# Kernel tuning notes

Hardware: AMD Instinct MI355X
Metric: run time of the kernel (lower is better)

Reference implementation:

```python
import jax, jax.numpy as jnp
import numpy as np

B, H, W = 128, 48, 48
CEN_IN, CEN_OUT, DIR_IN, DIR_OUT, CEN_K, DIR_K = 32, 32, 24, 24, 3, 5
C_IN = CEN_IN + 4 * DIR_IN  # central + 4 directional groups (hor, ver, diag, anti-diag)


def _dwconv(x, k):
    # x: [B, C, H, W], k: [C, kh, kw] depthwise kernels -> SAME-padded depthwise conv
    C = x.shape[1]
    return jax.lax.conv_general_dilated(
        x, k[:, None], window_strides=(1, 1), padding='SAME',
        dimension_numbers=('NCHW', 'OIHW', 'NCHW'), feature_group_count=C)


def setup_inputs() -> dict:
    key = jax.random.key(0)
    ks = jax.random.split(key, 8)
    s = 0.1
    return {
        'x': jax.random.normal(ks[0], (B, C_IN, H, W), dtype=jnp.float32),
        'cen_tensor': jax.random.normal(ks[1], (CEN_IN, CEN_K, CEN_K), dtype=jnp.float32) * s,
        'dir_tensor': jax.random.normal(ks[2], (DIR_IN, DIR_K), dtype=jnp.float32) * s,
        'cen2cen': jax.random.normal(ks[3], (CEN_OUT, CEN_IN), dtype=jnp.float32) * s,
        'par2cen': jax.random.normal(ks[4], (CEN_OUT, DIR_IN), dtype=jnp.float32) * s,
        'dia2cen': jax.random.normal(ks[5], (CEN_OUT, DIR_IN), dtype=jnp.float32) * s,
        'cen2dir': jax.random.normal(ks[6], (DIR_OUT, CEN_IN), dtype=jnp.float32) * s,
        'dir2dir': jax.random.normal(ks[7], (DIR_OUT, DIR_IN), dtype=jnp.float32) * s,
    }


def reference(x, cen_tensor, dir_tensor, cen2cen, par2cen, dia2cen, cen2dir, dir2dir):
    cen_in = cen_tensor.shape[0]
    dir_in, K = dir_tensor.shape
    # split channel groups: [cen | hor | ver | diag | anti-diag]
    xc = x[:, :cen_in]
    xh = x[:, cen_in:cen_in + dir_in]
    xv = x[:, cen_in + dir_in:cen_in + 2 * dir_in]
    xd1 = x[:, cen_in + 2 * dir_in:cen_in + 3 * dir_in]
    xd2 = x[:, cen_in + 3 * dir_in:]
    eye = jnp.eye(K, dtype=x.dtype)
    # --- directional depthwise stage ---
    yc = _dwconv(xc, cen_tensor)                                # full 2D kernel per channel
    yh = _dwconv(xh, dir_tensor[:, None, :])
    yv = _dwconv(xv, dir_tensor[:, :, None])                    # K x 1 vertical line
    yd1 = _dwconv(xd1, dir_tensor[:, :, None] * eye)            # main diagonal line
    yd2 = _dwconv(xd2, dir_tensor[:, :, None] * eye[:, ::-1])   # anti-diagonal line
    # --- directional pointwise (1x1) mixing stage ---
    mix = lambda Wm, t: jnp.einsum('oc,bchw->bohw', Wm, t)
    out_cen = mix(cen2cen, yc) + mix(par2cen, yh + yv) + mix(dia2cen, yd1 + yd2)
    od_cen = mix(cen2dir, yc)
    out_dirs = [od_cen + mix(dir2dir, t) for t in (yh, yv, yd1, yd2)]
    return jnp.concatenate([out_cen] + out_dirs, axis=1)
```

## Files before the change

kernel.cpp:

```cpp
#include <hip/hip_runtime.h>
#include <hip/hip_bf16.h>


namespace {
constexpr int HH = 48, WW = 48, HW = HH * WW;
constexpr int C_IN = 128, C_OUT = 128, NB = 128;
constexpr int RPB = 8;
constexpr int NSTR = HH / RPB;
constexpr int PIX = RPB * WW;
constexpr int NT = 512;
constexpr int CHK = 8;
constexpr int NCHK = C_IN / CHK;
constexpr int XR = RPB + 4;
constexpr int QR = 17;
constexpr int XQ = CHK * XR * QR;
constexpr int XROWF = QR * 4;
constexpr int YCS = 392;
constexpr size_t M_BYTES = 128 * 128 * 2;
constexpr size_t ZB_OFF = M_BYTES;
}

typedef __attribute__((ext_vector_type(8))) short bf16x8;
typedef __attribute__((ext_vector_type(4))) float f32x4;

__device__ __forceinline__ ushort f2bf(float f) {
    __hip_bfloat16 h = __float2bfloat16(f);
    return *reinterpret_cast<ushort*>(&h);
}

__global__ void build_M(const float* __restrict__ c2c, const float* __restrict__ p2c,
                        const float* __restrict__ d2c, const float* __restrict__ c2d,
                        const float* __restrict__ d2dW, ushort* __restrict__ Mbf) {
    int t = blockIdx.x * 256 + threadIdx.x;
    if (t >= 128 * 128) return;
    int o = t & 127, c = t >> 7;
    float v;
    if (o < 32) {
        if (c < 32)       v = c2c[o * 32 + c];
        else if (c < 56)  v = p2c[o * 24 + c - 32];
        else if (c < 80)  v = p2c[o * 24 + c - 56];
        else if (c < 104) v = d2c[o * 24 + c - 80];
        else              v = d2c[o * 24 + c - 104];
    } else {
        int g = (o - 32) / 24, oo = (o - 32) % 24;
        if (c < 32) v = c2d[oo * 32 + c];
        else {
            int gc = (c - 32) / 24, cc2 = (c - 32) % 24;
            v = (gc == g) ? d2dW[oo * 24 + cc2] : 0.f;
        }
    }
    Mbf[o * 128 + c] = f2bf(v);
}

__global__ __launch_bounds__(NT) void dsc_fused(
    const float* __restrict__ x,
    const float* __restrict__ cen_t,
    const float* __restrict__ dir_t,
    const ushort* __restrict__ Mbf,
    const float* __restrict__ zb,
    float* __restrict__ out)
{
    __shared__ float  xs[2][XQ * 4];
    __shared__ ushort yT[PIX * 128];
    __shared__ ushort ycp[2][CHK * YCS];

    const int tid = threadIdx.x;
    const int b   = blockIdx.x / NSTR;
    const int h0  = (blockIdx.x % NSTR) * RPB;
    const float* __restrict__ xb = x + (size_t)b * C_IN * HW;

    auto stage = [&](int t, int buf) {
        const int c0 = t * CHK;
#pragma unroll
        for (int k = 0; k < 4; ++k) {
            int d = tid + k * NT;
            if (d < XQ) {
                int q  = d % QR;
                int cr = d / QR;
                int r  = cr % XR;
                int c  = cr / XR;
                int gh = h0 - 2 + r;
                bool ok = ((unsigned)gh < (unsigned)HH) && (q < 12);
                const float* src = ok ? (xb + (size_t)(c0 + c) * HW + gh * WW + q * 4) : zb;
                __builtin_amdgcn_global_load_lds(
                    (const __attribute__((address_space(1))) unsigned int*)src,
                    (__attribute__((address_space(3))) unsigned int*)(&xs[buf][0] + (size_t)d * 4),
                    16, 0, 0);
            }
        }
    };

    auto dwconv = [&](int t) {
        const int c0 = t * CHK;
        const int buf = t & 1;
        ushort* yc = ycp[buf];
#pragma unroll
        for (int k = 0; k < 3; ++k) {
            int task = tid + k * NT;
            int c   = task / 192;
            int pt  = task % 192;
            int row = pt / 24;
            int w0  = (pt % 24) * 2;
            int cc  = c0 + c;
            const float* xb0 = &xs[buf][(size_t)(c * XR) * XROWF];
            float a0 = 0.f, a1 = 0.f;
            if (cc < 32) {
#pragma unroll
                for (int i = 0; i < 3; ++i) {
                    const float* xr = xb0 + (row + 1 + i) * XROWF;
                    float v0 = xr[(w0 - 1) & 63];
                    float v1 = xr[w0];
                    float v2 = xr[w0 + 1];
                    float v3 = xr[(w0 + 2) & 63];
                    float k0 = cen_t[cc * 9 + i * 3 + 0];
                    float k1 = cen_t[cc * 9 + i * 3 + 1];
                    float k2 = cen_t[cc * 9 + i * 3 + 2];
                    a0 += k0 * v0 + k1 * v1 + k2 * v2;
                    a1 += k0 * v1 + k1 * v2 + k2 * v3;
                }
            } else if (cc < 56) {
                int cd = cc - 32;
                const float* xr = xb0 + (row + 2) * XROWF;
                float v[6];
#pragma unroll
                for (int m = 0; m < 6; ++m) v[m] = xr[(w0 + m - 2) & 63];
#pragma unroll
                for (int i = 0; i < 5; ++i) {
                    float tt = dir_t[cd * 5 + i];
                    a0 += tt * v[i];
                    a1 += tt * v[i + 1];
                }
            } else if (cc < 80) {
                int cd = cc - 56;
#pragma unroll
                for (int i = 0; i < 5; ++i) {
                    float tt = dir_t[cd * 5 + i];
                    float2 vq = *(const float2*)(xb0 + (row + i) * XROWF + w0);
                    a0 += tt * vq.x;
                    a1 += tt * vq.y;
                }
            } else if (cc < 104) {
                int cd = cc - 80;
#pragma unroll
                for (int i = 0; i < 5; ++i) {
                    float tt = dir_t[cd * 5 + i];
                    const float* xr = xb0 + (row + i) * XROWF;
                    a0 += tt * xr[(w0 + i - 2) & 63];
                    a1 += tt * xr[(w0 + i - 1) & 63];
                }
            } else {
                int cd = cc - 104;
#pragma unroll
                for (int i = 0; i < 5; ++i) {
                    float tt = dir_t[cd * 5 + i];
                    const float* xr = xb0 + (row + i) * XROWF;
                    a0 += tt * xr[(w0 + 2 - i) & 63];
                    a1 += tt * xr[(w0 + 3 - i) & 63];
                }
            }
            ushort2 s = {f2bf(a0), f2bf(a1)};
            *(ushort2*)&yc[c * YCS + pt * 2] = s;
        }
    };

    auto transpose = [&](int t) {
        const ushort* src = ycp[t & 1];
#pragma unroll
        for (int k = 0; k < 3; ++k) {
            int task = tid + k * NT;
            int cp = task & 3;
            int p  = task >> 2;
            ushort2 s;
            s.x = src[(cp * 2 + 0) * YCS + p];
            s.y = src[(cp * 2 + 1) * YCS + p];
            int gsw = t ^ (p & 7);
            *(ushort2*)((char*)yT + p * 256 + (gsw << 4) + (cp << 2)) = s;
        }
    };

    stage(0, 0);
    __syncthreads();
    for (int t = 0; t < NCHK; ++t) {
        if (t + 1 < NCHK) stage(t + 1, (t + 1) & 1);
        dwconv(t);
        if (t > 0) transpose(t - 1);
        __syncthreads();
    }
    transpose(NCHK - 1);
    __syncthreads();

    const int l     = tid & 63;
    const int wv    = tid >> 6;
    const int ofr   = wv & 3;
    const int phalf = wv >> 2;
    float* __restrict__ ob = out + (size_t)b * C_OUT * HW + h0 * WW;

#pragma unroll
    for (int pass = 0; pass < 2; ++pass) {
        int o0 = pass * 64 + ofr * 16;
        bf16x8 afr[4];
#pragma unroll
        for (int kb = 0; kb < 4; ++kb)
            afr[kb] = *(const bf16x8*)(Mbf + (o0 + (l & 15)) * 128 + kb * 32 + (l >> 4) * 8);
        f32x4 acc[12] = {};
#pragma unroll
        for (int kb = 0; kb < 4; ++kb) {
            int g = kb * 4 + (l >> 4);
#pragma unroll
            for (int pf = 0; pf < 12; ++pf) {
                int p = (phalf * 12 + pf) * 16 + (l & 15);
                const bf16x8 bfr = *(const bf16x8*)((const char*)yT + p * 256 + ((g ^ (p & 7)) << 4));
                acc[pf] = __builtin_amdgcn_mfma_f32_16x16x32_bf16(afr[kb], bfr, acc[pf], 0, 0, 0);
            }
        }
#pragma unroll
        for (int pf = 0; pf < 12; ++pf) {
            int p = (phalf * 12 + pf) * 16 + (l & 15);
            int obase = o0 + (l >> 4) * 4;
#pragma unroll
            for (int r = 0; r < 4; ++r)
                ob[(size_t)(obase + r) * HW + p] = acc[pf][r];
        }
    }
}

extern "C" void kernel_launch(void* const* d_in, const int* in_sizes, int n_in,
                              void* d_out, int out_size, void* d_ws, size_t ws_size,
                              hipStream_t stream) {
    const float* x     = (const float*)d_in[0];
    const float* cen_t = (const float*)d_in[1];
    const float* dir_t = (const float*)d_in[2];
    const float* c2c   = (const float*)d_in[3];
    const float* p2c   = (const float*)d_in[4];
    const float* d2c   = (const float*)d_in[5];
    const float* c2d   = (const float*)d_in[6];
    const float* d2dW  = (const float*)d_in[7];
    float* out = (float*)d_out;

    ushort* Mbf = (ushort*)d_ws;
    float*  zb  = (float*)((char*)d_ws + ZB_OFF);

    hipMemsetAsync(zb, 0, 64, stream);
    build_M<<<64, 256, 0, stream>>>(c2c, p2c, d2c, c2d, d2dW, Mbf);
    dsc_fused<<<NB * NSTR, NT, 0, stream>>>(x, cen_t, dir_t, Mbf, zb, out);
}
```

Measured before the change: 117.5 us.

## Single-buffer larger channel chunks with 8-wide vectorized depthwise conv

Doubles the channel chunk size to 16 and drops the double-buffered input and dwconv staging tiles in favour of single buffers. Each thread now computes 8 contiguous output pixels using float4 LDS window loads. The transpose now writes full 16-byte groups. Staging of the next chunk now overlaps only with the transpose, and each iteration needs two barriers instead of one. The schedule is less overlapped than before in exchange for fewer iterations, wider LDS accesses, and possibly a smaller LDS footprint.

```diff
diff --git a/kernel.cpp b/kernel.cpp
--- a/kernel.cpp
+++ b/kernel.cpp
@@ -9,12 +9,12 @@
 constexpr int NSTR = HH / RPB;
 constexpr int PIX = RPB * WW;
 constexpr int NT = 512;
-constexpr int CHK = 8;
+constexpr int CHK = 16;
 constexpr int NCHK = C_IN / CHK;
 constexpr int XR = RPB + 4;
 constexpr int QR = 17;
+constexpr int XROWF = QR * 4;
 constexpr int XQ = CHK * XR * QR;
-constexpr int XROWF = QR * 4;
 constexpr int YCS = 392;
 constexpr size_t M_BYTES = 128 * 128 * 2;
 constexpr size_t ZB_OFF = M_BYTES;
@@ -60,19 +60,19 @@
     const float* __restrict__ zb,
     float* __restrict__ out)
 {
-    __shared__ float  xs[2][XQ * 4];
+    __shared__ float  xs[XQ * 4];
     __shared__ ushort yT[PIX * 128];
-    __shared__ ushort ycp[2][CHK * YCS];
+    __shared__ ushort ycp[CHK * YCS];
 
     const int tid = threadIdx.x;
     const int b   = blockIdx.x / NSTR;
     const int h0  = (blockIdx.x % NSTR) * RPB;
     const float* __restrict__ xb = x + (size_t)b * C_IN * HW;
 
-    auto stage = [&](int t, int buf) {
+    auto stage = [&](int t) {
         const int c0 = t * CHK;
 #pragma unroll
-        for (int k = 0; k < 4; ++k) {
+        for (int k = 0; k < 7; ++k) {
             int d = tid + k * NT;
             if (d < XQ) {
                 int q  = d % QR;
@@ -84,7 +84,7 @@
                 const float* src = ok ? (xb + (size_t)(c0 + c) * HW + gh * WW + q * 4) : zb;
                 __builtin_amdgcn_global_load_lds(
                     (const __attribute__((address_space(1))) unsigned int*)src,
-                    (__attribute__((address_space(3))) unsigned int*)(&xs[buf][0] + (size_t)d * 4),
+                    (__attribute__((address_space(3))) unsigned int*)(xs + (size_t)d * 4),
                     16, 0, 0);
             }
         }
@@ -92,102 +92,119 @@
 
     auto dwconv = [&](int t) {
         const int c0 = t * CHK;
-        const int buf = t & 1;
-        ushort* yc = ycp[buf];
-#pragma unroll
-        for (int k = 0; k < 3; ++k) {
+#pragma unroll
+        for (int k = 0; k < 2; ++k) {
             int task = tid + k * NT;
-            int c   = task / 192;
-            int pt  = task % 192;
-            int row = pt / 24;
-            int w0  = (pt % 24) * 2;
+            if (task >= CHK * 48) break;
+            int c   = task / 48;
+            int pg  = task % 48;
+            int row = pg & 7;
+            int w0  = (pg >> 3) * 8;
             int cc  = c0 + c;
-            const float* xb0 = &xs[buf][(size_t)(c * XR) * XROWF];
-            float a0 = 0.f, a1 = 0.f;
+            const float* xr0 = xs + (size_t)(c * XR) * XROWF;
+            float acc[8];
+#pragma unroll
+            for (int j = 0; j < 8; ++j) acc[j] = 0.f;
+
             if (cc < 32) {
 #pragma unroll
                 for (int i = 0; i < 3; ++i) {
-                    const float* xr = xb0 + (row + 1 + i) * XROWF;
-                    float v0 = xr[(w0 - 1) & 63];
-                    float v1 = xr[w0];
-                    float v2 = xr[w0 + 1];
-                    float v3 = xr[(w0 + 2) & 63];
-                    float k0 = cen_t[cc * 9 + i * 3 + 0];
-                    float k1 = cen_t[cc * 9 + i * 3 + 1];
-                    float k2 = cen_t[cc * 9 + i * 3 + 2];
-                    a0 += k0 * v0 + k1 * v1 + k2 * v2;
-                    a1 += k0 * v1 + k1 * v2 + k2 * v3;
+                    const float* xr = xr0 + (row + 1 + i) * XROWF;
+                    float4 A = *(const float4*)&xr[(w0 - 4) & 63];
+                    float4 B = *(const float4*)&xr[w0];
+                    float4 C = *(const float4*)&xr[w0 + 4];
+                    float4 D = *(const float4*)&xr[(w0 + 8) & 63];
+                    float win[16] = {A.x,A.y,A.z,A.w, B.x,B.y,B.z,B.w,
+                                     C.x,C.y,C.z,C.w, D.x,D.y,D.z,D.w};
+                    float k0 = cen_t[cc*9 + i*3 + 0];
+                    float k1 = cen_t[cc*9 + i*3 + 1];
+                    float k2 = cen_t[cc*9 + i*3 + 2];
+#pragma unroll
+                    for (int j = 0; j < 8; ++j)
+                        acc[j] += k0*win[j+3] + k1*win[j+4] + k2*win[j+5];
                 }
             } else if (cc < 56) {
                 int cd = cc - 32;
-                const float* xr = xb0 + (row + 2) * XROWF;
-                float v[6];
-#pragma unroll
-                for (int m = 0; m < 6; ++m) v[m] = xr[(w0 + m - 2) & 63];
+                const float* xr = xr0 + (row + 2) * XROWF;
+                float4 A = *(const float4*)&xr[(w0 - 4) & 63];
+                float4 B = *(const float4*)&xr[w0];
+                float4 C = *(const float4*)&xr[w0 + 4];
+                float4 D = *(const float4*)&xr[(w0 + 8) & 63];
+                float win[16] = {A.x,A.y,A.z,A.w, B.x,B.y,B.z,B.w,
+                                 C.x,C.y,C.z,C.w, D.x,D.y,D.z,D.w};
 #pragma unroll
                 for (int i = 0; i < 5; ++i) {
-                    float tt = dir_t[cd * 5 + i];
-                    a0 += tt * v[i];
-                    a1 += tt * v[i + 1];
+                    float tt = dir_t[cd*5 + i];
+#pragma unroll
+                    for (int j = 0; j < 8; ++j) acc[j] += tt * win[j+2+i];
                 }
             } else if (cc < 80) {
                 int cd = cc - 56;
 #pragma unroll
                 for (int i = 0; i < 5; ++i) {
-                    float tt = dir_t[cd * 5 + i];
-                    float2 vq = *(const float2*)(xb0 + (row + i) * XROWF + w0);
-                    a0 += tt * vq.x;
-                    a1 += tt * vq.y;
-                }
-            } else if (cc < 104) {
-                int cd = cc - 80;
+                    const float* xr = xr0 + (row + i) * XROWF;
+                    float4 B = *(const float4*)&xr[w0];
+                    float4 C = *(const float4*)&xr[w0 + 4];
+                    float w8[8] = {B.x,B.y,B.z,B.w, C.x,C.y,C.z,C.w};
+                    float tt = dir_t[cd*5 + i];
+#pragma unroll
+                    for (int j = 0; j < 8; ++j) acc[j] += tt * w8[j];
+                }
+            } else {
+                int cd  = (cc < 104) ? cc - 80 : cc - 104;
+                bool d1 = (cc < 104);
 #pragma unroll
                 for (int i = 0; i < 5; ++i) {
-                    float tt = dir_t[cd * 5 + i];
-                    const float* xr = xb0 + (row + i) * XROWF;
-                    a0 += tt * xr[(w0 + i - 2) & 63];
-                    a1 += tt * xr[(w0 + i - 1) & 63];
-                }
-            } else {
-                int cd = cc - 104;
-#pragma unroll
-                for (int i = 0; i < 5; ++i) {
-                    float tt = dir_t[cd * 5 + i];
-                    const float* xr = xb0 + (row + i) * XROWF;
-                    a0 += tt * xr[(w0 + 2 - i) & 63];
-                    a1 += tt * xr[(w0 + 3 - i) & 63];
+                    const float* xr = xr0 + (row + i) * XROWF;
+                    float4 A = *(const float4*)&xr[(w0 - 4) & 63];
+                    float4 B = *(const float4*)&xr[w0];
+                    float4 C = *(const float4*)&xr[w0 + 4];
+                    float4 D = *(const float4*)&xr[(w0 + 8) & 63];
+                    float win[16] = {A.x,A.y,A.z,A.w, B.x,B.y,B.z,B.w,
+                                     C.x,C.y,C.z,C.w, D.x,D.y,D.z,D.w};
+                    float tt = dir_t[cd*5 + i];
+                    if (d1) {
+#pragma unroll
+                        for (int j = 0; j < 8; ++j) acc[j] += tt * win[j+2+i];
+                    } else {
+#pragma unroll
+                        for (int j = 0; j < 8; ++j) acc[j] += tt * win[j+6-i];
+                    }
                 }
             }
-            ushort2 s = {f2bf(a0), f2bf(a1)};
-            *(ushort2*)&yc[c * YCS + pt * 2] = s;
+
+            union { ushort us[8]; uint4 v4; } s;
+#pragma unroll
+            for (int j = 0; j < 8; ++j) s.us[j] = f2bf(acc[j]);
+            *(uint4*)&ycp[c * YCS + row * 48 + w0] = s.v4;
         }
     };
 
     auto transpose = [&](int t) {
-        const ushort* src = ycp[t & 1];
-#pragma unroll
-        for (int k = 0; k < 3; ++k) {
+#pragma unroll
+        for (int k = 0; k < 2; ++k) {
             int task = tid + k * NT;
-            int cp = task & 3;
-            int p  = task >> 2;
-            ushort2 s;
-            s.x = src[(cp * 2 + 0) * YCS + p];
-            s.y = src[(cp * 2 + 1) * YCS + p];
-            int gsw = t ^ (p & 7);
-            *(ushort2*)((char*)yT + p * 256 + (gsw << 4) + (cp << 2)) = s;
+            if (task >= 2 * PIX) break;
+            int gg = task / PIX;
+            int p  = task % PIX;
+            int g  = t * 2 + gg;
+            union { ushort us[8]; uint4 v4; } s;
+#pragma unroll
+            for (int j = 0; j < 8; ++j) s.us[j] = ycp[(gg * 8 + j) * YCS + p];
+            int byte = p * 256 + ((g ^ (p & 7)) << 4);
+            *(uint4*)((char*)yT + byte) = s.v4;
         }
     };
 
-    stage(0, 0);
+    stage(0);
     __syncthreads();
     for (int t = 0; t < NCHK; ++t) {
-        if (t + 1 < NCHK) stage(t + 1, (t + 1) & 1);
         dwconv(t);
-        if (t > 0) transpose(t - 1);
+        __syncthreads();
+        if (t + 1 < NCHK) stage(t + 1);
+        transpose(t);
         __syncthreads();
     }
-    transpose(NCHK - 1);
-    __syncthreads();
 
     const int l     = tid & 63;
     const int wv    = tid >> 6;
```

After: 102.1 us. 1.15x faster.
